# Kernel tuning notes

Hardware: AMD Instinct MI355X
Metric: run time of the kernel (lower is better)

## Reference

```python
import jax, jax.numpy as jnp
import numpy as np

B, T, D, H = 2, 2048, 2048, 16
HS = D // H  # head size 128


def setup_inputs() -> dict:
    key = jax.random.key(0)
    ks = jax.random.split(key, 5)
    s = 0.02
    return {
        "x": jax.random.normal(ks[0], (B, T, D), dtype=jnp.float32),
        "wq": jax.random.normal(ks[1], (D, D), dtype=jnp.float32) * s,
        "wk": jax.random.normal(ks[2], (D, D), dtype=jnp.float32) * s,
        "wv": jax.random.normal(ks[3], (D, D), dtype=jnp.float32) * s,
        "wo": jax.random.normal(ks[4], (D, D), dtype=jnp.float32) * s,
    }


def reference(x, wq, wk, wv, wo):
    b, t, d = x.shape
    # projections: nn.Linear(x) = x @ W.T ; here W stored as (out,in)
    q = (x @ wq.T).reshape(b, t, H, HS).transpose(0, 2, 1, 3)  # (B,H,T,HS)
    k = (x @ wk.T).reshape(b, t, H, HS).transpose(0, 2, 1, 3)
    v = (x @ wv.T).reshape(b, t, H, HS).transpose(0, 2, 1, 3)
    scale = 1.0 / np.sqrt(HS).astype(np.float32)
    e = jnp.einsum("bhqd,bhkd->bhqk", q, k) * scale  # (B,H,T,T)
    causal = jnp.tril(jnp.ones((t, t), dtype=bool))
    e = jnp.where(causal[None, None], e, jnp.float32(-jnp.inf))
    alpha = jax.nn.softmax(e, axis=-1)  # dropout=0.0 -> identity
    attn = jnp.einsum("bhqk,bhkd->bhqd", alpha, v)
    attn = attn.transpose(0, 2, 1, 3).reshape(b, t, d)
    return attn @ wo.T
```

## Files before the change

kernel.cpp:

```cpp
#include <hip/hip_runtime.h>
#include <hip/hip_bf16.h>

typedef __bf16 bf16x8 __attribute__((ext_vector_type(8)));
typedef float f32x4 __attribute__((ext_vector_type(4)));
typedef unsigned short u16x8 __attribute__((ext_vector_type(8)));

#define GLDS16(g, s)                                                         \
  __builtin_amdgcn_global_load_lds(                                          \
      (const __attribute__((address_space(1))) void*)(g),                    \
      (__attribute__((address_space(3))) void*)(s), 16, 0, 0)

__device__ __forceinline__ void store1(__hip_bfloat16* p, float v) { *p = __float2bfloat16(v); }
__device__ __forceinline__ void store1(float* p, float v) { *p = v; }

__global__ __launch_bounds__(256) void cast_f32_to_bf16(const float4* __restrict__ in,
                                                        ushort4* __restrict__ out, int n4) {
  int i = blockIdx.x * 256 + threadIdx.x;
  if (i >= n4) return;
  float4 v = in[i];
  union { ushort4 u; __hip_bfloat16 h[4]; } o;
  o.h[0] = __float2bfloat16(v.x);
  o.h[1] = __float2bfloat16(v.y);
  o.h[2] = __float2bfloat16(v.z);
  o.h[3] = __float2bfloat16(v.w);
  out[i] = o.u;
}

template <typename OutT>
__global__ __launch_bounds__(512, 2) void gemm256(const __hip_bfloat16* __restrict__ A,
                                                  const __hip_bfloat16* __restrict__ B0,
                                                  const __hip_bfloat16* __restrict__ B1,
                                                  const __hip_bfloat16* __restrict__ B2,
                                                  OutT* __restrict__ C0,
                                                  OutT* __restrict__ C1,
                                                  OutT* __restrict__ C2,
                                                  int nBx, int nBy, int ntPerMat,
                                                  int N, int K) {
  __shared__ __hip_bfloat16 As[2][256 * 64];
  __shared__ __hip_bfloat16 Bs[2][256 * 64];

  const int t = threadIdx.x;
  const int w = t >> 6, l = t & 63;
  const int lr = l & 15, hi = l >> 4;

  const int nwg = nBx * nBy;
  int id = (int)blockIdx.x;
  id = (id & 7) * (nwg >> 3) + (id >> 3);
  const int bx = id % nBx;
  const int by = id / nBx;

  const int sel = bx / ntPerMat;
  const __hip_bfloat16* Bm = (sel == 0) ? B0 : ((sel == 1) ? B1 : B2);
  OutT* Cm = (sel == 0) ? C0 : ((sel == 1) ? C1 : C2);
  const int n0 = (bx - sel * ntPerMat) * 256;
  const int m0 = by * 256;

  const int c0r = t >> 3, cs = t & 7;
  const int c1r = 64 + c0r;
  const __hip_bfloat16* aP0 = A + (size_t)(m0 + c0r) * K + (cs ^ (c0r & 7)) * 8;
  const __hip_bfloat16* aP1 = A + (size_t)(m0 + c1r) * K + (cs ^ (c1r & 7)) * 8;
  const __hip_bfloat16* bP0 = Bm + (size_t)(n0 + c0r) * K + (cs ^ (c0r & 7)) * 8;
  const __hip_bfloat16* bP1 = Bm + (size_t)(n0 + c1r) * K + (cs ^ (c1r & 7)) * 8;
  const size_t HK = (size_t)128 * K;

#define STAGE_S(sidx, nb, koff)                                              \
  do {                                                                       \
    if ((sidx) == 0) {                                                       \
      GLDS16(aP0 + (koff), (char*)As[nb] + t * 16);                          \
      GLDS16(aP1 + (koff), (char*)As[nb] + 8192 + t * 16);                   \
    } else if ((sidx) == 1) {                                                \
      GLDS16(bP0 + (koff), (char*)Bs[nb] + t * 16);                          \
      GLDS16(bP1 + (koff), (char*)Bs[nb] + 8192 + t * 16);                   \
    } else if ((sidx) == 2) {                                                \
      GLDS16(aP0 + HK + (koff), (char*)As[nb] + 16384 + t * 16);             \
      GLDS16(aP1 + HK + (koff), (char*)As[nb] + 24576 + t * 16);             \
    } else {                                                                 \
      GLDS16(bP0 + HK + (koff), (char*)Bs[nb] + 16384 + t * 16);             \
      GLDS16(bP1 + HK + (koff), (char*)Bs[nb] + 24576 + t * 16);             \
    }                                                                        \
  } while (0)

  f32x4 acc[2][2][4][2] = {};
  const int NT = K / 64;
  const int sw = lr & 7;

#define PHASE(mh, nh, sidx)                                                  \
  do {                                                                       \
    asm volatile("s_waitcnt vmcnt(4)" ::: "memory");                         \
    __builtin_amdgcn_s_barrier();                                            \
    const char* as_ = (const char*)As[buf];                                  \
    const char* bs_ = (const char*)Bs[buf];                                  \
    bf16x8 af[4][2], bq[2][2];                                               \
    _Pragma("unroll") for (int mi = 0; mi < 4; ++mi)                         \
      _Pragma("unroll") for (int kk = 0; kk < 2; ++kk)                       \
        af[mi][kk] = *(const bf16x8*)(as_ +                                  \
            ((mh) * 128 + (w >> 2) * 64 + mi * 16 + lr) * 128 +              \
            (((kk * 4 + hi) ^ sw) << 4));                                    \
    _Pragma("unroll") for (int ni = 0; ni < 2; ++ni)                         \
      _Pragma("unroll") for (int kk = 0; kk < 2; ++kk)                       \
        bq[ni][kk] = *(const bf16x8*)(bs_ +                                  \
            ((nh) * 128 + (w & 3) * 32 + ni * 16 + lr) * 128 +               \
            (((kk * 4 + hi) ^ sw) << 4));                                    \
    if (tt + 1 < NT) STAGE_S((sidx), nb, (size_t)(tt + 1) * 64);             \
    __builtin_amdgcn_s_setprio(1);                                           \
    _Pragma("unroll") for (int mi = 0; mi < 4; ++mi)                         \
      _Pragma("unroll") for (int ni = 0; ni < 2; ++ni) {                     \
        acc[mh][nh][mi][ni] = __builtin_amdgcn_mfma_f32_16x16x32_bf16(       \
            af[mi][0], bq[ni][0], acc[mh][nh][mi][ni], 0, 0, 0);             \
        acc[mh][nh][mi][ni] = __builtin_amdgcn_mfma_f32_16x16x32_bf16(       \
            af[mi][1], bq[ni][1], acc[mh][nh][mi][ni], 0, 0, 0);             \
      }                                                                      \
    __builtin_amdgcn_s_setprio(0);                                           \
  } while (0)

  STAGE_S(0, 0, 0);
  STAGE_S(1, 0, 0);
  STAGE_S(2, 0, 0);
  STAGE_S(3, 0, 0);

  for (int tt = 0; tt < NT; ++tt) {
    const int buf = tt & 1, nb = buf ^ 1;
    PHASE(0, 0, 0);
    PHASE(1, 0, 1);
    PHASE(0, 1, 2);
    PHASE(1, 1, 3);
  }
#undef PHASE
#undef STAGE_S

#pragma unroll
  for (int mh = 0; mh < 2; ++mh)
#pragma unroll
    for (int nh = 0; nh < 2; ++nh)
#pragma unroll
      for (int mi = 0; mi < 4; ++mi)
#pragma unroll
        for (int ni = 0; ni < 2; ++ni)
#pragma unroll
          for (int i = 0; i < 4; ++i) {
            size_t idx = (size_t)(m0 + mh * 128 + (w >> 2) * 64 + mi * 16 + hi * 4 + i) * N +
                         (n0 + nh * 128 + (w & 3) * 32 + ni * 16 + lr);
            store1(&Cm[idx], acc[mh][nh][mi][ni][i]);
          }
}

__global__ __launch_bounds__(256, 2) void flash_attn(const __hip_bfloat16* __restrict__ Qg,
                                                     const __hip_bfloat16* __restrict__ Kg,
                                                     const __hip_bfloat16* __restrict__ Vg,
                                                     __hip_bfloat16* __restrict__ Og) {
  __shared__ __hip_bfloat16 Ks[2][64 * 128];
  __shared__ __hip_bfloat16 Vt[128 * 64];

  const int mblk = blockIdx.x;
  const int bh = mblk & 31;
  const int jj = mblk >> 5;
  const int qt = (jj < 8) ? (15 - jj) : (jj - 8);
  const int b = bh >> 4, h = bh & 15;
  const int q0 = qt * 128;
  const int t = threadIdx.x, w = t >> 6, l = t & 63;
  const int lr = l & 15, hi = l >> 4;
  const size_t base = ((size_t)b * 2048) * 2048 + (size_t)h * 128;
  const int nt = 2 * qt + 2;
  const float scale = 0.08838834764831843f;

  const int hi2 = (hi & 1) * 2;
  const int addrA = (((hi2) << 4) | lr) << 2;
  const int addrB = (((hi2 + 1) << 4) | lr) << 2;
  int addr_o[4];
#pragma unroll
  for (int i = 0; i < 4; ++i) addr_o[i] = ((l & 48) | (hi * 4 + i)) << 2;
  const bool hiHigh = (hi >> 1) != 0;

  bf16x8 qf[2][4];
#pragma unroll
  for (int g = 0; g < 2; ++g) {
    const __hip_bfloat16* qrow = Qg + base + (size_t)(q0 + w * 32 + g * 16 + lr) * 2048;
#pragma unroll
    for (int kk = 0; kk < 4; ++kk)
      qf[g][kk] = *(const bf16x8*)(qrow + kk * 32 + hi * 8);
  }

  f32x4 o_acc[2][8] = {};
  float m_run[2] = {-1e30f, -1e30f};
  float l_run[2] = {0.f, 0.f};

  const __hip_bfloat16* kptr[4];
#pragma unroll
  for (int i = 0; i < 4; ++i) {
    int c = i * 256 + t;
    int kr = c >> 4;
    int ke = ((c & 15) ^ (kr & 7)) * 8;
    kptr[i] = Kg + base + (size_t)kr * 2048 + ke;
  }
  const __hip_bfloat16* vptr[2];
#pragma unroll
  for (int it = 0; it < 2; ++it) {
    int kp = it * 16 + w * 4 + hi;
    vptr[it] = Vg + base + (size_t)(kp * 2) * 2048 + lr * 8;
  }

  u16x8 va[2], vb[2];
#pragma unroll
  for (int i = 0; i < 4; ++i)
    GLDS16(kptr[i], (char*)Ks[0] + (i * 256 + t) * 16);
#pragma unroll
  for (int it = 0; it < 2; ++it) {
    va[it] = *(const u16x8*)vptr[it];
    vb[it] = *(const u16x8*)(vptr[it] + 2048);
  }

  for (int kt = 0; kt < nt; ++kt) {
    const int cur = kt & 1;
    const int kb = kt * 64;
    __syncthreads();

#pragma unroll
    for (int it = 0; it < 2; ++it)
#pragma unroll
      for (int j2 = 0; j2 < 8; ++j2) {
        int d = lr * 8 + j2;
        int sw = (lr ^ j2) & 7;
        int off = d * 128 + (((it * 4 + w) ^ sw) << 4) + hi * 4;
        *(unsigned int*)((char*)Vt + off) =
            (unsigned int)va[it][j2] | ((unsigned int)vb[it][j2] << 16);
      }
    if (kt + 1 < nt) {
      const size_t adv = (size_t)(kb + 64) * 2048;
#pragma unroll
      for (int i = 0; i < 4; ++i)
        GLDS16(kptr[i] + adv, (char*)Ks[cur ^ 1] + (i * 256 + t) * 16);
#pragma unroll
      for (int it = 0; it < 2; ++it) {
        va[it] = *(const u16x8*)(vptr[it] + adv);
        vb[it] = *(const u16x8*)(vptr[it] + adv + 2048);
      }
    }
    asm volatile("s_waitcnt lgkmcnt(0)" ::: "memory");
    __builtin_amdgcn_s_barrier();

    if (!(kt == nt - 1 && w < 2)) {
      const char* ks = (const char*)Ks[cur];

      f32x4 st[2][4];
#pragma unroll
      for (int g = 0; g < 2; ++g)
#pragma unroll
        for (int nk = 0; nk < 4; ++nk) { f32x4 z = {}; st[g][nk] = z; }
#pragma unroll
      for (int nk = 0; nk < 4; ++nk)
#pragma unroll
        for (int kk = 0; kk < 4; ++kk) {
          bf16x8 kf = *(const bf16x8*)(ks + (nk * 16 + lr) * 256 +
                                       (((kk * 4 + hi) ^ (lr & 7)) << 4));
#pragma unroll
          for (int g = 0; g < 2; ++g)
            st[g][nk] = __builtin_amdgcn_mfma_f32_16x16x32_bf16(kf, qf[g][kk], st[g][nk], 0, 0, 0);
        }

      const bool maskt = (kt >= nt - 2);
#pragma unroll
      for (int g = 0; g < 2; ++g)
#pragma unroll
        for (int nk = 0; nk < 4; ++nk)
#pragma unroll
          for (int i = 0; i < 4; ++i) {
            float v = st[g][nk][i] * scale;
            if (maskt) {
              int ki = kb + nk * 16 + hi * 4 + i;
              int qi = q0 + w * 32 + g * 16 + lr;
              if (ki > qi) v = -1e30f;
            }
            st[g][nk][i] = v;
          }

      bf16x8 paf[2][2];
#pragma unroll
      for (int g = 0; g < 2; ++g) {
        float t0 = fmaxf(fmaxf(st[g][0][0], st[g][0][1]), fmaxf(st[g][0][2], st[g][0][3]));
        float t1 = fmaxf(fmaxf(st[g][1][0], st[g][1][1]), fmaxf(st[g][1][2], st[g][1][3]));
        float t2 = fmaxf(fmaxf(st[g][2][0], st[g][2][1]), fmaxf(st[g][2][2], st[g][2][3]));
        float t3 = fmaxf(fmaxf(st[g][3][0], st[g][3][1]), fmaxf(st[g][3][2], st[g][3][3]));
        float mx = fmaxf(fmaxf(t0, t1), fmaxf(t2, t3));
        mx = fmaxf(mx, __shfl_xor(mx, 16));
        mx = fmaxf(mx, __shfl_xor(mx, 32));

        if (!__all(mx - m_run[g] <= 8.0f)) {
          float mnew = fmaxf(m_run[g], mx);
          float rs = __expf(m_run[g] - mnew);
          m_run[g] = mnew;
          l_run[g] *= rs;
          int rsi = __float_as_int(rs);
#pragma unroll
          for (int i = 0; i < 4; ++i) {
            float rso = __int_as_float(__builtin_amdgcn_ds_bpermute(addr_o[i], rsi));
#pragma unroll
            for (int nc = 0; nc < 8; ++nc) o_acc[g][nc][i] *= rso;
          }
        }

#pragma unroll
        for (int nk = 0; nk < 4; ++nk)
#pragma unroll
          for (int i = 0; i < 4; ++i)
            st[g][nk][i] = __expf(st[g][nk][i] - m_run[g]);

        float s0 = (st[g][0][0] + st[g][0][1]) + (st[g][0][2] + st[g][0][3]);
        float s1 = (st[g][1][0] + st[g][1][1]) + (st[g][1][2] + st[g][1][3]);
        float s2 = (st[g][2][0] + st[g][2][1]) + (st[g][2][2] + st[g][2][3]);
        float s3 = (st[g][3][0] + st[g][3][1]) + (st[g][3][2] + st[g][3][3]);
        float sm = (s0 + s1) + (s2 + s3);
        sm += __shfl_xor(sm, 16);
        sm += __shfl_xor(sm, 32);
        l_run[g] += sm;

        unsigned pk[4][2];
#pragma unroll
        for (int nk = 0; nk < 4; ++nk) {
          asm("v_cvt_pk_bf16_f32 %0, %1, %2"
              : "=v"(pk[nk][0]) : "v"(st[g][nk][0]), "v"(st[g][nk][1]));
          asm("v_cvt_pk_bf16_f32 %0, %1, %2"
              : "=v"(pk[nk][1]) : "v"(st[g][nk][2]), "v"(st[g][nk][3]));
        }

#pragma unroll
        for (int kk = 0; kk < 2; ++kk) {
          unsigned au[4];
#pragma unroll
          for (int p = 0; p < 4; ++p) {
            int ad = (p < 2) ? addrA : addrB;
            int v0 = __builtin_amdgcn_ds_bpermute(ad, (int)pk[2 * kk][p & 1]);
            int v1 = __builtin_amdgcn_ds_bpermute(ad, (int)pk[2 * kk + 1][p & 1]);
            au[p] = hiHigh ? (unsigned)v1 : (unsigned)v0;
          }
          union { unsigned u[4]; bf16x8 v; } cv;
          cv.u[0] = au[0]; cv.u[1] = au[1]; cv.u[2] = au[2]; cv.u[3] = au[3];
          paf[g][kk] = cv.v;
        }
      }

#pragma unroll
      for (int kk = 0; kk < 2; ++kk)
#pragma unroll
        for (int nc = 0; nc < 8; ++nc) {
          int d = nc * 16 + lr;
          int sw = ((d >> 3) ^ d) & 7;
          bf16x8 vfr = *(const bf16x8*)((const char*)Vt + d * 128 +
                                        (((kk * 4 + hi) ^ sw) << 4));
#pragma unroll
          for (int g = 0; g < 2; ++g)
            o_acc[g][nc] = __builtin_amdgcn_mfma_f32_16x16x32_bf16(paf[g][kk], vfr, o_acc[g][nc], 0, 0, 0);
        }
    }
  }

#pragma unroll
  for (int g = 0; g < 2; ++g) {
    float lo[4];
#pragma unroll
    for (int i = 0; i < 4; ++i)
      lo[i] = __int_as_float(__builtin_amdgcn_ds_bpermute(addr_o[i], __float_as_int(l_run[g])));
#pragma unroll
    for (int nc = 0; nc < 8; ++nc)
#pragma unroll
      for (int i = 0; i < 4; ++i) {
        float val = o_acc[g][nc][i] / lo[i];
        Og[base + (size_t)(q0 + w * 32 + g * 16 + hi * 4 + i) * 2048 + nc * 16 + lr] =
            __float2bfloat16(val);
      }
  }
}

extern "C" void kernel_launch(void* const* d_in, const int* in_sizes, int n_in,
                              void* d_out, int out_size, void* d_ws, size_t ws_size,
                              hipStream_t stream) {
  const float* x  = (const float*)d_in[0];
  const float* wq = (const float*)d_in[1];
  const float* wk = (const float*)d_in[2];
  const float* wv = (const float*)d_in[3];
  const float* wo = (const float*)d_in[4];
  float* out = (float*)d_out;

  const int BT = 4096, D = 2048;
  const size_t ND = (size_t)D * D;
  const size_t NX = (size_t)BT * D;

  __hip_bfloat16* xb  = (__hip_bfloat16*)d_ws;
  __hip_bfloat16* wqb = xb + NX;
  __hip_bfloat16* wkb = wqb + ND;
  __hip_bfloat16* wvb = wkb + ND;
  __hip_bfloat16* wob = wvb + ND;
  __hip_bfloat16* Qb  = wob + ND;
  __hip_bfloat16* Kb  = Qb + NX;
  __hip_bfloat16* Vb  = Kb + NX;
  __hip_bfloat16* Ab  = Vb + NX;

  cast_f32_to_bf16<<<(int)(NX / 4 / 256), 256, 0, stream>>>((const float4*)x,  (ushort4*)xb,  (int)(NX / 4));
  cast_f32_to_bf16<<<(int)(ND / 4 / 256), 256, 0, stream>>>((const float4*)wq, (ushort4*)wqb, (int)(ND / 4));
  cast_f32_to_bf16<<<(int)(ND / 4 / 256), 256, 0, stream>>>((const float4*)wk, (ushort4*)wkb, (int)(ND / 4));
  cast_f32_to_bf16<<<(int)(ND / 4 / 256), 256, 0, stream>>>((const float4*)wv, (ushort4*)wvb, (int)(ND / 4));
  cast_f32_to_bf16<<<(int)(ND / 4 / 256), 256, 0, stream>>>((const float4*)wo, (ushort4*)wob, (int)(ND / 4));

  gemm256<__hip_bfloat16><<<384, 512, 0, stream>>>(xb, wqb, wkb, wvb, Qb, Kb, Vb,
                                                   24, 16, 8, D, D);

  flash_attn<<<512, 256, 0, stream>>>(Qb, Kb, Vb, Ab);

  gemm256<float><<<128, 512, 0, stream>>>(Ab, wob, wob, wob, out, out, out,
                                          8, 16, 8, D, D);
}
```

Baseline: 302.0 us.

## Reorder GEMM quadrant phases to reuse LDS fragments and reorder tile mapping

Restructures the 256x256 GEMM main loop so the four quadrant phases run in a snake order (00,01,11,10). A and B register fragments loaded from LDS are kept and reused across phases, roughly halving LDS reads per k-step. The staging order of the global-to-LDS loads is permuted to match, and the last iteration waits with vmcnt(0). Workgroup-to-tile mapping switches from row-major to column-major over the grid, which changes L2 reuse patterns. It also raises register pressure by holding two B fragment sets at once.

```diff
diff --git a/kernel.cpp b/kernel.cpp
--- a/kernel.cpp
+++ b/kernel.cpp
@@ -46,8 +46,8 @@
   const int nwg = nBx * nBy;
   int id = (int)blockIdx.x;
   id = (id & 7) * (nwg >> 3) + (id >> 3);
-  const int bx = id % nBx;
-  const int by = id / nBx;
+  const int bx = id / nBy;
+  const int by = id % nBy;
 
   const int sel = bx / ntPerMat;
   const __hip_bfloat16* Bm = (sel == 0) ? B0 : ((sel == 1) ? B1 : B2);
@@ -81,27 +81,25 @@
   } while (0)
 
   f32x4 acc[2][2][4][2] = {};
+  bf16x8 af[4][2];
+  bf16x8 bqA[2][2], bqB[2][2];
   const int NT = K / 64;
   const int sw = lr & 7;
-
-#define PHASE(mh, nh, sidx)                                                  \
+  const int arow = (w >> 2) * 64;
+  const int brow = (w & 3) * 32;
+
+#define LOAD_A(mh)                                                           \
+  _Pragma("unroll") for (int mi = 0; mi < 4; ++mi)                           \
+    _Pragma("unroll") for (int kk = 0; kk < 2; ++kk)                         \
+      af[mi][kk] = *(const bf16x8*)((const char*)As[buf] +                   \
+          ((mh) * 128 + arow + mi * 16 + lr) * 128 + (((kk * 4 + hi) ^ sw) << 4));
+#define LOAD_B(dst, nh)                                                      \
+  _Pragma("unroll") for (int ni = 0; ni < 2; ++ni)                           \
+    _Pragma("unroll") for (int kk = 0; kk < 2; ++kk)                         \
+      dst[ni][kk] = *(const bf16x8*)((const char*)Bs[buf] +                  \
+          ((nh) * 128 + brow + ni * 16 + lr) * 128 + (((kk * 4 + hi) ^ sw) << 4));
+#define MFMA_Q(mh, nh, bq)                                                   \
   do {                                                                       \
-    asm volatile("s_waitcnt vmcnt(4)" ::: "memory");                         \
-    __builtin_amdgcn_s_barrier();                                            \
-    const char* as_ = (const char*)As[buf];                                  \
-    const char* bs_ = (const char*)Bs[buf];                                  \
-    bf16x8 af[4][2], bq[2][2];                                               \
-    _Pragma("unroll") for (int mi = 0; mi < 4; ++mi)                         \
-      _Pragma("unroll") for (int kk = 0; kk < 2; ++kk)                       \
-        af[mi][kk] = *(const bf16x8*)(as_ +                                  \
-            ((mh) * 128 + (w >> 2) * 64 + mi * 16 + lr) * 128 +              \
-            (((kk * 4 + hi) ^ sw) << 4));                                    \
-    _Pragma("unroll") for (int ni = 0; ni < 2; ++ni)                         \
-      _Pragma("unroll") for (int kk = 0; kk < 2; ++kk)                       \
-        bq[ni][kk] = *(const bf16x8*)(bs_ +                                  \
-            ((nh) * 128 + (w & 3) * 32 + ni * 16 + lr) * 128 +               \
-            (((kk * 4 + hi) ^ sw) << 4));                                    \
-    if (tt + 1 < NT) STAGE_S((sidx), nb, (size_t)(tt + 1) * 64);             \
     __builtin_amdgcn_s_setprio(1);                                           \
     _Pragma("unroll") for (int mi = 0; mi < 4; ++mi)                         \
       _Pragma("unroll") for (int ni = 0; ni < 2; ++ni) {                     \
@@ -112,20 +110,47 @@
       }                                                                      \
     __builtin_amdgcn_s_setprio(0);                                           \
   } while (0)
+#define WAITB(lastt)                                                         \
+  do {                                                                       \
+    if (lastt) asm volatile("s_waitcnt vmcnt(0)" ::: "memory");              \
+    else       asm volatile("s_waitcnt vmcnt(4)" ::: "memory");              \
+    __builtin_amdgcn_s_barrier();                                            \
+  } while (0)
 
   STAGE_S(0, 0, 0);
   STAGE_S(1, 0, 0);
+  STAGE_S(3, 0, 0);
   STAGE_S(2, 0, 0);
-  STAGE_S(3, 0, 0);
 
   for (int tt = 0; tt < NT; ++tt) {
     const int buf = tt & 1, nb = buf ^ 1;
-    PHASE(0, 0, 0);
-    PHASE(1, 0, 1);
-    PHASE(0, 1, 2);
-    PHASE(1, 1, 3);
-  }
-#undef PHASE
+    const bool stg = (tt + 1 < NT);
+    const bool lastt = !stg;
+    const size_t ko = (size_t)(tt + 1) * 64;
+
+    WAITB(lastt);
+    LOAD_A(0); LOAD_B(bqA, 0);
+    if (stg) STAGE_S(0, nb, ko);
+    MFMA_Q(0, 0, bqA);
+
+    WAITB(lastt);
+    LOAD_B(bqB, 1);
+    if (stg) STAGE_S(1, nb, ko);
+    MFMA_Q(0, 1, bqB);
+
+    WAITB(lastt);
+    LOAD_A(1);
+    if (stg) STAGE_S(3, nb, ko);
+    MFMA_Q(1, 1, bqB);
+
+    WAITB(lastt);
+    if (stg) STAGE_S(2, nb, ko);
+    MFMA_Q(1, 0, bqA);
+  }
+#undef WAITB
+#undef MFMA_Q
+#undef LOAD_B
+#undef LOAD_A
 #undef STAGE_S
 
 #pragma unroll
@@ -138,8 +163,8 @@
         for (int ni = 0; ni < 2; ++ni)
 #pragma unroll
           for (int i = 0; i < 4; ++i) {
-            size_t idx = (size_t)(m0 + mh * 128 + (w >> 2) * 64 + mi * 16 + hi * 4 + i) * N +
-                         (n0 + nh * 128 + (w & 3) * 32 + ni * 16 + lr);
+            size_t idx = (size_t)(m0 + mh * 128 + arow + mi * 16 + hi * 4 + i) * N +
+                         (n0 + nh * 128 + brow + ni * 16 + lr);
             store1(&Cm[idx], acc[mh][nh][mi][ni][i]);
           }
 }
```

Result: faster. 291.8 us (-3.4%).
